# Performance work log

Measured on AMD Instinct MI355X. Metric: run time of the kernel, lower is better.

## Reference

```python
import jax, jax.numpy as jnp
import numpy as np

B, N, E, F = 8, 16384, 64, 64


def euler_zyx_to_matrix(J):
    # J: [..., 3] euler angles (alpha about Z, beta about Y, gamma about X)
    # R = Rz(alpha) @ Ry(beta) @ Rx(gamma)  (pytorch3d 'ZYX' convention)
    a, b, g = J[..., 0], J[..., 1], J[..., 2]
    ca, sa = jnp.cos(a), jnp.sin(a)
    cb, sb = jnp.cos(b), jnp.sin(b)
    cg, sg = jnp.cos(g), jnp.sin(g)
    r00 = ca * cb
    r01 = ca * sb * sg - sa * cg
    r02 = ca * sb * cg + sa * sg
    r10 = sa * cb
    r11 = sa * sb * sg + ca * cg
    r12 = sa * sb * cg - ca * sg
    r20 = -sb
    r21 = cb * sg
    r22 = cb * cg
    R = jnp.stack([
        jnp.stack([r00, r01, r02], axis=-1),
        jnp.stack([r10, r11, r12], axis=-1),
        jnp.stack([r20, r21, r22], axis=-1),
    ], axis=-2)  # [..., 3, 3]
    return R


def setup_inputs() -> dict:
    key = jax.random.key(0)
    k1, k2, k3, k4, k5 = jax.random.split(key, 5)
    X = jax.random.normal(k1, (B, N, E, 3), dtype=jnp.float32)
    J = jax.random.uniform(k2, (B, N, E, 3), dtype=jnp.float32)
    A = jax.random.normal(k3, (F, E), dtype=jnp.float32)
    Bw = jax.random.normal(k4, (F, E), dtype=jnp.float32)
    C = jax.random.normal(k5, (F, E), dtype=jnp.float32)
    return {"X": X, "J": J, "A": A, "Bw": Bw, "C": C}


def reference(X, J, A, Bw, C):
    R = euler_zyx_to_matrix(J)                 # [B, N, E, 3, 3]
    # v = R^T X  (per-point 3-vector): v_i = sum_k R[..., k, i] * X[..., k]
    v = jnp.einsum('bneki,bnek->bnei', R, X)   # [B, N, E, 3]
    col0 = R[..., :, 0]                        # [B, N, E, 3]
    col1 = R[..., :, 1]
    col2 = R[..., :, 2]
    v0 = v[..., 0:1]
    v1 = v[..., 1:2]
    v2 = v[..., 2:3]
    a_term = col0 * v0 + col1 * v1             # [B, N, E, 3]
    b_term = col1 * v0 - col0 * v1
    c_term = col2 * v2
    Y = (jnp.einsum('fe,bnei->bnfi', A, a_term)
         + jnp.einsum('fe,bnei->bnfi', Bw, b_term)
         + jnp.einsum('fe,bnei->bnfi', C, c_term))
    return Y
```

## Files before the change

kernel.cpp:

```cpp
#include <hip/hip_runtime.h>


#define NPOS   131072
#define PB     16
#define NC     (PB * 3)
#define ITERS  4
#define BLOCKS 2048
#define THREADS 256
#define PPW    4

typedef _Float16 half8 __attribute__((ext_vector_type(8)));
typedef float floatx4 __attribute__((ext_vector_type(4)));

__global__ __launch_bounds__(THREADS, 4)
void fused_mfma(const float* __restrict__ X, const float* __restrict__ J,
                const float* __restrict__ A, const float* __restrict__ Bw,
                const float* __restrict__ Cm, float* __restrict__ Y) {
    __shared__ _Float16 Tl[6][NC][4][8];
    __shared__ float Ys[PB * 192];

    const int lane = threadIdx.x & 63;
    const int w    = threadIdx.x >> 6;
    const int tid  = threadIdx.x;

    const int fa  = w * 16 + (lane & 15);
    const int kgA = lane >> 4;
    half8 afrag[6];
    #pragma unroll
    for (int ks = 0; ks < 6; ++ks) {
        const float* mat = (ks < 2) ? A : (ks < 4 ? Bw : Cm);
        const float* src = mat + fa * 64 + (ks & 1) * 32 + kgA * 8;
        float4 lo = *(const float4*)src;
        float4 hi = *(const float4*)(src + 4);
        half8 h;
        h[0] = (_Float16)lo.x; h[1] = (_Float16)lo.y;
        h[2] = (_Float16)lo.z; h[3] = (_Float16)lo.w;
        h[4] = (_Float16)hi.x; h[5] = (_Float16)hi.y;
        h[6] = (_Float16)hi.z; h[7] = (_Float16)hi.w;
        afrag[ks] = h;
    }

    const int ks0 = lane >> 5;
    const int kgW = (lane & 31) >> 3;
    const int jW  = lane & 7;
    const int kgR = (lane >> 4) ^ (((lane & 15) >> 1) & 3);

    float jr[PPW][3], xr[PPW][3];

    auto LOAD = [&](int it) {
        #pragma unroll
        for (int q = 0; q < PPW; ++q) {
            const int p = (blockIdx.x * ITERS + it) * PB + w * PPW + q;
            const float* jp = J + (size_t)(p * 64 + lane) * 3;
            const float* xp = X + (size_t)(p * 64 + lane) * 3;
            jr[q][0] = jp[0]; jr[q][1] = jp[1]; jr[q][2] = jp[2];
            xr[q][0] = xp[0]; xr[q][1] = xp[1]; xr[q][2] = xp[2];
        }
    };

    auto P1 = [&]() {
        #pragma unroll
        for (int q = 0; q < PPW; ++q) {
            const int p_local = w * PPW + q;
            float ja = jr[q][0], jb = jr[q][1], jg = jr[q][2];
            float x0 = xr[q][0], x1 = xr[q][1], x2 = xr[q][2];
            float sa, ca, sb, cb, sg, cg;
            __sincosf(ja, &sa, &ca);
            __sincosf(jb, &sb, &cb);
            __sincosf(jg, &sg, &cg);
            float casb = ca * sb, sasb = sa * sb;
            float r00 = ca * cb, r01 = casb * sg - sa * cg, r02 = casb * cg + sa * sg;
            float r10 = sa * cb, r11 = sasb * sg + ca * cg, r12 = sasb * cg - ca * sg;
            float r20 = -sb,     r21 = cb * sg,             r22 = cb * cg;
            float v0 = fmaf(r00, x0, fmaf(r10, x1, r20 * x2));
            float v1 = fmaf(r01, x0, fmaf(r11, x1, r21 * x2));
            float v2 = fmaf(r02, x0, fmaf(r12, x1, r22 * x2));
            float ta[3], tb[3], tc[3];
            ta[0] = fmaf(r00, v0, r01 * v1);
            ta[1] = fmaf(r10, v0, r11 * v1);
            ta[2] = fmaf(r20, v0, r21 * v1);
            tb[0] = fmaf(r01, v0, -r00 * v1);
            tb[1] = fmaf(r11, v0, -r10 * v1);
            tb[2] = fmaf(r21, v0, -r20 * v1);
            tc[0] = r02 * v2; tc[1] = r12 * v2; tc[2] = r22 * v2;

            #pragma unroll
            for (int i = 0; i < 3; ++i) {
                const int n  = p_local * 3 + i;
                const int kg = kgW ^ ((n >> 1) & 3);
                Tl[0 + ks0][n][kg][jW] = (_Float16)ta[i];
                Tl[2 + ks0][n][kg][jW] = (_Float16)tb[i];
                Tl[4 + ks0][n][kg][jW] = (_Float16)tc[i];
            }
        }
    };

    auto P2 = [&]() {
        #pragma unroll
        for (int nt = 0; nt < 3; ++nt) {
            floatx4 acc = {0.f, 0.f, 0.f, 0.f};
            #pragma unroll
            for (int ks = 0; ks < 6; ++ks) {
                half8 b = *(const half8*)&Tl[ks][nt * 16 + (lane & 15)][kgR][0];
                acc = __builtin_amdgcn_mfma_f32_16x16x32_f16(afrag[ks], b, acc, 0, 0, 0);
            }
            const int n = nt * 16 + (lane & 15);
            const int pl2 = (n * 171) >> 9;
            const int i2  = n - pl2 * 3;
            const int fbase = w * 16 + (lane >> 4) * 4;
            #pragma unroll
            for (int r = 0; r < 4; ++r)
                Ys[pl2 * 192 + (fbase + r) * 3 + i2] = acc[r];
        }
    };

    auto STORE_Y = [&](int it) {
        float* yb = Y + (size_t)(blockIdx.x * ITERS + it) * PB * 192;
        #pragma unroll
        for (int k = 0; k < 3; ++k) {
            const int d = (tid + 256 * k) * 4;
            floatx4 v = *(const floatx4*)&Ys[d];
            __builtin_nontemporal_store(v.x, &yb[d + 0]);
            __builtin_nontemporal_store(v.y, &yb[d + 1]);
            __builtin_nontemporal_store(v.z, &yb[d + 2]);
            __builtin_nontemporal_store(v.w, &yb[d + 3]);
        }
    };

    LOAD(0);
    P1();
    for (int t = 0; t < ITERS; ++t) {
        __syncthreads();
        if (t + 1 < ITERS) LOAD(t + 1);
        P2();
        __syncthreads();
        STORE_Y(t);
        if (t + 1 < ITERS) P1();
    }
}

extern "C" void kernel_launch(void* const* d_in, const int* in_sizes, int n_in,
                              void* d_out, int out_size, void* d_ws, size_t ws_size,
                              hipStream_t stream) {
    const float* X  = (const float*)d_in[0];
    const float* J  = (const float*)d_in[1];
    const float* A  = (const float*)d_in[2];
    const float* Bw = (const float*)d_in[3];
    const float* Cm = (const float*)d_in[4];
    float* Y = (float*)d_out;
    fused_mfma<<<BLOCKS, THREADS, 0, stream>>>(X, J, A, Bw, Cm, Y);
}
```

Measured before the change: 56.14 us.

## Restructure into single-wave blocks holding all F tiles, dropping block barriers

Each block becomes one 64-thread wave that keeps all four 16-row F tiles of the A/Bw/C weights in registers. Each wave processes 4 positions per iteration, with a single shared B fragment feeding four MFMAs per k-step. That removes the __syncthreads barriers, since LDS is only shared within one wave. The padded 16-column tile wastes 4 of 16 columns, and register pressure rises from the 24 A fragments. The Y staging buffer gets an XOR swizzle to cut LDS bank conflicts, and output is written with 16-byte vector nontemporal stores.

```diff
diff --git a/kernel.cpp b/kernel.cpp
--- a/kernel.cpp
+++ b/kernel.cpp
@@ -2,42 +2,41 @@
 
 
 #define NPOS   131072
-#define PB     16
-#define NC     (PB * 3)
-#define ITERS  4
-#define BLOCKS 2048
-#define THREADS 256
 #define PPW    4
+#define ITERS  8
+#define BLOCKS (NPOS / (PPW * ITERS))
+#define THREADS 64
 
 typedef _Float16 half8 __attribute__((ext_vector_type(8)));
 typedef float floatx4 __attribute__((ext_vector_type(4)));
 
-__global__ __launch_bounds__(THREADS, 4)
-void fused_mfma(const float* __restrict__ X, const float* __restrict__ J,
+__global__ __launch_bounds__(THREADS, 2)
+void fused_wave(const float* __restrict__ X, const float* __restrict__ J,
                 const float* __restrict__ A, const float* __restrict__ Bw,
                 const float* __restrict__ Cm, float* __restrict__ Y) {
-    __shared__ _Float16 Tl[6][NC][4][8];
-    __shared__ float Ys[PB * 192];
+    __shared__ _Float16 Tl[6][16][4][8];
+    __shared__ float Ys[PPW * 192];
 
-    const int lane = threadIdx.x & 63;
-    const int w    = threadIdx.x >> 6;
-    const int tid  = threadIdx.x;
+    const int lane = threadIdx.x;
 
-    const int fa  = w * 16 + (lane & 15);
+    const int fr  = lane & 15;
     const int kgA = lane >> 4;
-    half8 afrag[6];
+    half8 afrag[4][6];
     #pragma unroll
-    for (int ks = 0; ks < 6; ++ks) {
-        const float* mat = (ks < 2) ? A : (ks < 4 ? Bw : Cm);
-        const float* src = mat + fa * 64 + (ks & 1) * 32 + kgA * 8;
-        float4 lo = *(const float4*)src;
-        float4 hi = *(const float4*)(src + 4);
-        half8 h;
-        h[0] = (_Float16)lo.x; h[1] = (_Float16)lo.y;
-        h[2] = (_Float16)lo.z; h[3] = (_Float16)lo.w;
-        h[4] = (_Float16)hi.x; h[5] = (_Float16)hi.y;
-        h[6] = (_Float16)hi.z; h[7] = (_Float16)hi.w;
-        afrag[ks] = h;
+    for (int ft = 0; ft < 4; ++ft) {
+        #pragma unroll
+        for (int ks = 0; ks < 6; ++ks) {
+            const float* mat = (ks < 2) ? A : (ks < 4 ? Bw : Cm);
+            const float* src = mat + (ft * 16 + fr) * 64 + (ks & 1) * 32 + kgA * 8;
+            float4 lo = *(const float4*)src;
+            float4 hi = *(const float4*)(src + 4);
+            half8 h;
+            h[0] = (_Float16)lo.x; h[1] = (_Float16)lo.y;
+            h[2] = (_Float16)lo.z; h[3] = (_Float16)lo.w;
+            h[4] = (_Float16)hi.x; h[5] = (_Float16)hi.y;
+            h[6] = (_Float16)hi.z; h[7] = (_Float16)hi.w;
+            afrag[ft][ks] = h;
+        }
     }
 
     const int ks0 = lane >> 5;
@@ -45,12 +44,14 @@
     const int jW  = lane & 7;
     const int kgR = (lane >> 4) ^ (((lane & 15) >> 1) & 3);
 
+    const int p0 = blockIdx.x * (PPW * ITERS);
+
     float jr[PPW][3], xr[PPW][3];
 
-    auto LOAD = [&](int it) {
+    auto LOAD = [&](int t) {
         #pragma unroll
         for (int q = 0; q < PPW; ++q) {
-            const int p = (blockIdx.x * ITERS + it) * PB + w * PPW + q;
+            const int p = p0 + t * PPW + q;
             const float* jp = J + (size_t)(p * 64 + lane) * 3;
             const float* xp = X + (size_t)(p * 64 + lane) * 3;
             jr[q][0] = jp[0]; jr[q][1] = jp[1]; jr[q][2] = jp[2];
@@ -61,7 +62,6 @@
     auto P1 = [&]() {
         #pragma unroll
         for (int q = 0; q < PPW; ++q) {
-            const int p_local = w * PPW + q;
             float ja = jr[q][0], jb = jr[q][1], jg = jr[q][2];
             float x0 = xr[q][0], x1 = xr[q][1], x2 = xr[q][2];
             float sa, ca, sb, cb, sg, cg;
@@ -86,7 +86,7 @@
 
             #pragma unroll
             for (int i = 0; i < 3; ++i) {
-                const int n  = p_local * 3 + i;
+                const int n  = q * 3 + i;
                 const int kg = kgW ^ ((n >> 1) & 3);
                 Tl[0 + ks0][n][kg][jW] = (_Float16)ta[i];
                 Tl[2 + ks0][n][kg][jW] = (_Float16)tb[i];
@@ -96,46 +96,51 @@
     };
 
     auto P2 = [&]() {
+        floatx4 acc[4];
         #pragma unroll
-        for (int nt = 0; nt < 3; ++nt) {
-            floatx4 acc = {0.f, 0.f, 0.f, 0.f};
+        for (int ft = 0; ft < 4; ++ft) acc[ft] = (floatx4){0.f, 0.f, 0.f, 0.f};
+        #pragma unroll
+        for (int ks = 0; ks < 6; ++ks) {
+            half8 b = *(const half8*)&Tl[ks][lane & 15][kgR][0];
             #pragma unroll
-            for (int ks = 0; ks < 6; ++ks) {
-                half8 b = *(const half8*)&Tl[ks][nt * 16 + (lane & 15)][kgR][0];
-                acc = __builtin_amdgcn_mfma_f32_16x16x32_f16(afrag[ks], b, acc, 0, 0, 0);
-            }
-            const int n = nt * 16 + (lane & 15);
+            for (int ft = 0; ft < 4; ++ft)
+                acc[ft] = __builtin_amdgcn_mfma_f32_16x16x32_f16(afrag[ft][ks], b, acc[ft], 0, 0, 0);
+        }
+        const int n = lane & 15;
+        if (n < 12) {
             const int pl2 = (n * 171) >> 9;
             const int i2  = n - pl2 * 3;
-            const int fbase = w * 16 + (lane >> 4) * 4;
             #pragma unroll
-            for (int r = 0; r < 4; ++r)
-                Ys[pl2 * 192 + (fbase + r) * 3 + i2] = acc[r];
+            for (int ft = 0; ft < 4; ++ft) {
+                const int f0 = ft * 16 + (lane >> 4) * 4;
+                #pragma unroll
+                for (int r = 0; r < 4; ++r) {
+                    const int z  = pl2 * 192 + (f0 + r) * 3 + i2;
+                    const int c  = z >> 2;
+                    const int zp = (((c ^ ((c >> 4) & 15))) << 2) | (z & 3);
+                    Ys[zp] = acc[ft][r];
+                }
+            }
         }
     };
 
-    auto STORE_Y = [&](int it) {
-        float* yb = Y + (size_t)(blockIdx.x * ITERS + it) * PB * 192;
+    auto STORE_Y = [&](int t) {
+        float* yb = Y + (size_t)(p0 + t * PPW) * 192;
         #pragma unroll
         for (int k = 0; k < 3; ++k) {
-            const int d = (tid + 256 * k) * 4;
-            floatx4 v = *(const floatx4*)&Ys[d];
-            __builtin_nontemporal_store(v.x, &yb[d + 0]);
-            __builtin_nontemporal_store(v.y, &yb[d + 1]);
-            __builtin_nontemporal_store(v.z, &yb[d + 2]);
-            __builtin_nontemporal_store(v.w, &yb[d + 3]);
+            const int c  = lane + 64 * k;
+            const int cp = c ^ ((c >> 4) & 15);
+            floatx4 v = *(const floatx4*)&Ys[cp * 4];
+            __builtin_nontemporal_store(v, (floatx4*)(yb + (size_t)c * 4));
         }
     };
 
     LOAD(0);
-    P1();
     for (int t = 0; t < ITERS; ++t) {
-        __syncthreads();
+        P1();
         if (t + 1 < ITERS) LOAD(t + 1);
         P2();
-        __syncthreads();
         STORE_Y(t);
-        if (t + 1 < ITERS) P1();
     }
 }
 
@@ -148,5 +153,5 @@
     const float* Bw = (const float*)d_in[3];
     const float* Cm = (const float*)d_in[4];
     float* Y = (float*)d_out;
-    fused_mfma<<<BLOCKS, THREADS, 0, stream>>>(X, J, A, Bw, Cm, Y);
+    fused_wave<<<BLOCKS, THREADS, 0, stream>>>(X, J, A, Bw, Cm, Y);
 }
```

Measured after the change: 64.17 us. 14.3% more time.
